# Optimization experiments

Hardware: AMD Instinct MI355X
Metric: run time of the kernel (lower is better)

## Reference

```python
import jax, jax.numpy as jnp
import numpy as np

B, S, D, H, DFF, V, LAT, L = 64, 256, 512, 8, 2048, 128, 512, 6
MAXLEN = 256
NEG = -1e9
EPS = 1e-5


def setup_inputs() -> dict:
    key = jax.random.key(0)
    ks = jax.random.split(key, 32)
    s = 0.02
    rn = lambda k, shape: jax.random.normal(k, shape, jnp.float32) * s
    inp = {
        "z": jax.random.normal(ks[0], (B, LAT), jnp.float32),
        "tgt_seq": jax.random.randint(ks[1], (B, S), 0, V),
        "emb": rn(ks[2], (V, D)).at[0].set(0.0),  # padding_idx=0 row zeroed
        "pos": rn(ks[3], (MAXLEN, D)),
        "proj_w": rn(ks[4], (D, LAT)),
        "proj_b": jnp.zeros((D,), jnp.float32),
        "sa_w": rn(ks[5], (L, 3 * D, D)),
        "sa_b": jnp.zeros((L, 3 * D), jnp.float32),
        "sa_ow": rn(ks[6], (L, D, D)),
        "sa_ob": jnp.zeros((L, D), jnp.float32),
        "ca_w": rn(ks[7], (L, 3 * D, D)),
        "ca_b": jnp.zeros((L, 3 * D), jnp.float32),
        "ca_ow": rn(ks[8], (L, D, D)),
        "ca_ob": jnp.zeros((L, D), jnp.float32),
        "ln1_s": jnp.ones((L, D), jnp.float32),
        "ln1_b": jnp.zeros((L, D), jnp.float32),
        "ln2_s": jnp.ones((L, D), jnp.float32),
        "ln2_b": jnp.zeros((L, D), jnp.float32),
        "ln3_s": jnp.ones((L, D), jnp.float32),
        "ln3_b": jnp.zeros((L, D), jnp.float32),
        "ff1_w": rn(ks[9], (L, DFF, D)),
        "ff1_b": jnp.zeros((L, DFF), jnp.float32),
        "ff2_w": rn(ks[10], (L, D, DFF)),
        "ff2_b": jnp.zeros((L, D), jnp.float32),
        "fc_w": rn(ks[11], (V, D)),
        "fc_b": jnp.zeros((V,), jnp.float32),
    }
    return inp


def _ln(x, s, b):
    m = jnp.mean(x, -1, keepdims=True)
    v = jnp.mean(jnp.square(x - m), -1, keepdims=True)
    return (x - m) * jax.lax.rsqrt(v + EPS) * s + b


def _mha(q_in, k_in, v_in, w, b, ow, ob, mask=None):
    # torch MultiheadAttention: packed in_proj [3D, D], out_proj [D, D]
    wq, wk, wv = w[:D], w[D:2 * D], w[2 * D:]
    bq, bk, bv = b[:D], b[D:2 * D], b[2 * D:]
    dh = D // H
    split = lambda t: t.reshape(t.shape[0], t.shape[1], H, dh)
    q = split(q_in @ wq.T + bq)  # [B,Sq,H,dh]
    k = split(k_in @ wk.T + bk)  # [B,Sk,H,dh]
    v = split(v_in @ wv.T + bv)
    scores = jnp.einsum("bqhd,bkhd->bhqk", q, k) / np.sqrt(dh).astype(np.float32)
    if mask is not None:
        scores = scores + mask
    attn = jax.nn.softmax(scores, axis=-1)
    out = jnp.einsum("bhqk,bkhd->bqhd", attn, v).reshape(q_in.shape[0], q_in.shape[1], D)
    return out @ ow.T + ob


def reference(z, tgt_seq, emb, pos, proj_w, proj_b, sa_w, sa_b, sa_ow, sa_ob,
              ca_w, ca_b, ca_ow, ca_ob, ln1_s, ln1_b, ln2_s, ln2_b, ln3_s, ln3_b,
              ff1_w, ff1_b, ff2_w, ff2_b, fc_w, fc_b):
    # memory = proj(z), length-1 cross-attention memory: [B,1,D]
    mem = (z @ proj_w.T + proj_b)[:, None, :]
    seq_len = tgt_seq.shape[1]
    x = emb[tgt_seq] + pos[:seq_len][None]  # [B,S,D]
    causal = jnp.where(jnp.tril(jnp.ones((seq_len, seq_len), bool)), 0.0, NEG)
    for i in range(L):  # post-norm TransformerDecoderLayer (torch default)
        sa = _mha(x, x, x, sa_w[i], sa_b[i], sa_ow[i], sa_ob[i], causal)
        x = _ln(x + sa, ln1_s[i], ln1_b[i])
        ca = _mha(x, mem, mem, ca_w[i], ca_b[i], ca_ow[i], ca_ob[i])
        x = _ln(x + ca, ln2_s[i], ln2_b[i])
        ff = jax.nn.relu(x @ ff1_w[i].T + ff1_b[i]) @ ff2_w[i].T + ff2_b[i]
        x = _ln(x + ff, ln3_s[i], ln3_b[i])
    logits = x @ fc_w.T + fc_b  # [B,S,V]
    return logits
```

## Files before the change

### kernel.cpp

```cpp
#include <hip/hip_runtime.h>

typedef unsigned int uint;
typedef unsigned short ushort;

typedef __attribute__((ext_vector_type(8))) __bf16 bf16x8;
typedef __attribute__((ext_vector_type(4))) float f32x4;

#define B_ 64
#define S_ 256
#define D_ 512
#define H_ 8
#define DFF_ 2048
#define V_ 128
#define L_ 6
#define BS_ (B_ * S_)

__device__ __forceinline__ float blo(uint u) { return __uint_as_float(u << 16); }
__device__ __forceinline__ float bhi(uint u) { return __uint_as_float(u & 0xffff0000u); }
__device__ __forceinline__ float b2f(ushort u) { return __uint_as_float(((uint)u) << 16); }
__device__ __forceinline__ ushort f2b(float f) {
  uint u = __float_as_uint(f);
  return (ushort)((u + 0x7fffu + ((u >> 16) & 1u)) >> 16);
}
__device__ __forceinline__ uint pack2(float a, float b) {
  return (uint)f2b(a) | ((uint)f2b(b) << 16);
}

#define GLOAD16(gp, lp)                                                        \
  __builtin_amdgcn_global_load_lds(                                            \
      (const __attribute__((address_space(1))) void*)(gp),                     \
      (__attribute__((address_space(3))) void*)(lp), 16, 0, 0)

__global__ __launch_bounds__(256) void conv_kernel(const float* __restrict__ src,
                                                   ushort* __restrict__ dst) {
  size_t p = (size_t)blockIdx.x * 256 + threadIdx.x;
  float2 v = ((const float2*)src)[p];
  ((uint*)dst)[p] = pack2(v.x, v.y);
}

__global__ __launch_bounds__(256) void embed_kernel(
    const int* __restrict__ tgt, const float* __restrict__ emb,
    const float* __restrict__ pos, ushort* __restrict__ x16) {
  int p = blockIdx.x * 256 + threadIdx.x;
  int row = p >> 8;
  int d2 = p & 255;
  int s = row & (S_ - 1);
  int tok = tgt[row];
  float2 e = ((const float2*)emb)[tok * 256 + d2];
  float2 pp = ((const float2*)pos)[s * 256 + d2];
  ((uint*)x16)[p] = pack2(e.x + pp.x, e.y + pp.y);
}

template <int MODE>
__global__ __launch_bounds__(256) void gemm_bt(
    const ushort* __restrict__ A, const ushort* __restrict__ W,
    const float* __restrict__ bias, void* __restrict__ Cv, int N, int K,
    int As, int Ws, int Cs) {
  __shared__ ushort la[128 * 32];
  __shared__ ushort lb[128 * 32];
  const int tid = threadIdx.x;
  const int wv = tid >> 6, lane = tid & 63;
  const int m0 = blockIdx.y << 7, n0 = blockIdx.x << 7;
  const int wm = (wv >> 1) << 6, wn = (wv & 1) << 6;
  const int tr = lane & 15, tq = lane >> 4;

  const int lin0 = wv * 1024 + lane * 8;
  const int lin1 = lin0 + 512;
  const int am0 = lin0 >> 5, ac0 = lin0 & 31;
  const int am1 = lin1 >> 5, ac1 = lin1 & 31;

  const ushort* pa0 = A + (size_t)(m0 + am0) * As + ac0;
  const ushort* pa1 = A + (size_t)(m0 + am1) * As + ac1;
  const ushort* pb0 = W + (size_t)(n0 + am0) * Ws + ac0;
  const ushort* pb1 = W + (size_t)(n0 + am1) * Ws + ac1;
  ushort* la0 = &la[wv * 1024];
  ushort* la1 = &la[wv * 1024 + 512];
  ushort* lb0 = &lb[wv * 1024];
  ushort* lb1 = &lb[wv * 1024 + 512];

  f32x4 acc[4][4];
#pragma unroll
  for (int i = 0; i < 4; ++i)
#pragma unroll
    for (int j = 0; j < 4; ++j) acc[i][j] = (f32x4)(0.f);

  const int KT = K >> 5;
  for (int kt = 0; kt < KT; ++kt) {
    const int kb = kt << 5;
    GLOAD16(pa0 + kb, la0);
    GLOAD16(pa1 + kb, la1);
    GLOAD16(pb0 + kb, lb0);
    GLOAD16(pb1 + kb, lb1);
    __syncthreads();
    bf16x8 av[4], bv[4];
#pragma unroll
    for (int i = 0; i < 4; ++i)
      av[i] = *(const bf16x8*)&la[(wm + i * 16 + tr) * 32 + tq * 8];
#pragma unroll
    for (int j = 0; j < 4; ++j)
      bv[j] = *(const bf16x8*)&lb[(wn + j * 16 + tr) * 32 + tq * 8];
#pragma unroll
    for (int i = 0; i < 4; ++i)
#pragma unroll
      for (int j = 0; j < 4; ++j)
        acc[i][j] =
            __builtin_amdgcn_mfma_f32_16x16x32_bf16(av[i], bv[j], acc[i][j], 0, 0, 0);
    __syncthreads();
  }

#pragma unroll
  for (int j = 0; j < 4; ++j) {
    const int gn = n0 + wn + j * 16 + tr;
    float bj = 0.f;
    if (MODE != 2) bj = bias[gn];
    float scl = 1.f;
    if (MODE == 4) scl = (gn < 512) ? 0.18033688011112042f : 1.f;
#pragma unroll
    for (int i = 0; i < 4; ++i) {
      const int gmb = m0 + wm + i * 16 + tq * 4;
#pragma unroll
      for (int r = 0; r < 4; ++r) {
        const size_t idx = (size_t)(gmb + r) * Cs + gn;
        float v = acc[i][j][r] + bj;
        if (MODE == 1) v = fmaxf(v, 0.f);
        if (MODE == 4) v *= scl;
        if (MODE == 3)
          ((float*)Cv)[idx] = v;
        else if (MODE == 2) {
          ushort* C = (ushort*)Cv;
          C[idx] = f2b(b2f(C[idx]) + acc[i][j][r]);
        } else
          ((ushort*)Cv)[idx] = f2b(v);
      }
    }
  }
}

__global__ __launch_bounds__(256) void gemm_btf(
    const ushort* __restrict__ A0, long zA, const float* __restrict__ W0,
    long zW, const float* __restrict__ bias0, long zb, ushort* __restrict__ C0,
    long zC, int N, int K, int As, int Ws, int Cs) {
  const int zz = blockIdx.z;
  const ushort* A = A0 + zA * zz;
  const float* W = W0 + zW * zz;
  const float* bias = bias0 + zb * zz;
  ushort* C = C0 + zC * zz;

  __shared__ ushort la[128 * 32];
  __shared__ ushort lb[128 * 32];
  const int tid = threadIdx.x;
  const int wv = tid >> 6, lane = tid & 63;
  const int m0 = blockIdx.y << 7, n0 = blockIdx.x << 7;
  const int wm = (wv >> 1) << 6, wn = (wv & 1) << 6;
  const int tr = lane & 15, tq = lane >> 4;

  const int lin0 = wv * 1024 + lane * 8;
  const int lin1 = lin0 + 512;
  const int am0 = lin0 >> 5, ac0 = lin0 & 31;
  const int am1 = lin1 >> 5, ac1 = lin1 & 31;

  const ushort* pa0 = A + (size_t)(m0 + am0) * As + ac0;
  const ushort* pa1 = A + (size_t)(m0 + am1) * As + ac1;
  const float* pb0 = W + (size_t)(n0 + am0) * Ws + ac0;
  const float* pb1 = W + (size_t)(n0 + am1) * Ws + ac1;

  f32x4 acc[4][4];
#pragma unroll
  for (int i = 0; i < 4; ++i)
#pragma unroll
    for (int j = 0; j < 4; ++j) acc[i][j] = (f32x4)(0.f);

  const int KT = K >> 5;
  for (int kt = 0; kt < KT; ++kt) {
    const int kb = kt << 5;
    uint4 ra0 = *(const uint4*)(pa0 + kb);
    uint4 ra1 = *(const uint4*)(pa1 + kb);
    float4 f00 = *(const float4*)(pb0 + kb);
    float4 f01 = *(const float4*)(pb0 + kb + 4);
    float4 f10 = *(const float4*)(pb1 + kb);
    float4 f11 = *(const float4*)(pb1 + kb + 4);
    uint4 rb0 = make_uint4(pack2(f00.x, f00.y), pack2(f00.z, f00.w),
                           pack2(f01.x, f01.y), pack2(f01.z, f01.w));
    uint4 rb1 = make_uint4(pack2(f10.x, f10.y), pack2(f10.z, f10.w),
                           pack2(f11.x, f11.y), pack2(f11.z, f11.w));
    __syncthreads();
    *(uint4*)&la[lin0] = ra0;
    *(uint4*)&la[lin1] = ra1;
    *(uint4*)&lb[lin0] = rb0;
    *(uint4*)&lb[lin1] = rb1;
    __syncthreads();
    bf16x8 av[4], bv[4];
#pragma unroll
    for (int i = 0; i < 4; ++i)
      av[i] = *(const bf16x8*)&la[(wm + i * 16 + tr) * 32 + tq * 8];
#pragma unroll
    for (int j = 0; j < 4; ++j)
      bv[j] = *(const bf16x8*)&lb[(wn + j * 16 + tr) * 32 + tq * 8];
#pragma unroll
    for (int i = 0; i < 4; ++i)
#pragma unroll
      for (int j = 0; j < 4; ++j)
        acc[i][j] =
            __builtin_amdgcn_mfma_f32_16x16x32_bf16(av[i], bv[j], acc[i][j], 0, 0, 0);
  }

#pragma unroll
  for (int j = 0; j < 4; ++j) {
    const int gn = n0 + wn + j * 16 + tr;
    const float bj = bias[gn];
#pragma unroll
    for (int i = 0; i < 4; ++i) {
      const int gmb = m0 + wm + i * 16 + tq * 4;
#pragma unroll
      for (int r = 0; r < 4; ++r)
        C[(size_t)(gmb + r) * Cs + gn] = f2b(acc[i][j][r] + bj);
    }
  }
}

__global__ __launch_bounds__(128) void attn_mfma(ushort* __restrict__ qkv) {
  __shared__ ushort lk[64 * 72];
  __shared__ ushort lvT[64 * 72];
  __shared__ ushort lp[2 * 64 * 72];
  const int qp = blockIdx.x, h = blockIdx.y, b = blockIdx.z;
  const int tid = threadIdx.x;
  const int g = tid >> 6, lane = tid & 63;
  const int tr = lane & 15, tq = lane >> 4;
  const int qc = qp * 2 + g;
  const int q0 = qc << 6;
  ushort* myp = &lp[g * 64 * 72];

  bf16x8 qf[4][2];
#pragma unroll
  for (int i = 0; i < 4; ++i)
#pragma unroll
    for (int s = 0; s < 2; ++s)
      qf[i][s] = *(const bf16x8*)(qkv +
                                  (size_t)(b * 256 + q0 + i * 16 + tr) * 1536 +
                                  h * 64 + s * 32 + tq * 8);

  f32x4 o[4][4];
  float pl[4][4];
#pragma unroll
  for (int i = 0; i < 4; ++i)
#pragma unroll
    for (int j = 0; j < 4; ++j) {
      o[i][j] = (f32x4)(0.f);
      pl[i][j] = 0.f;
    }

  const int key = tid >> 1, half = tid & 1;
  const int cmax = qp * 2 + 1;
  for (int c = 0; c <= cmax; ++c) {
    __syncthreads();
    const ushort* gk =
        qkv + (size_t)(b * 256 + c * 64 + key) * 1536 + 512 + h * 64 + half * 32;
#pragma unroll
    for (int u = 0; u < 4; ++u)
      *(uint4*)&lk[key * 72 + half * 32 + u * 8] = *(const uint4*)(gk + u * 8);
    ushort vloc[32];
#pragma unroll
    for (int u = 0; u < 4; ++u)
      *(uint4*)&vloc[u * 8] = *(const uint4*)(gk + 512 + u * 8);
#pragma unroll
    for (int dd = 0; dd < 32; ++dd)
      lvT[(half * 32 + dd) * 72 + key] = vloc[dd];
    __syncthreads();

    if (c <= qc) {
      f32x4 Sv[4][4];
#pragma unroll
      for (int i = 0; i < 4; ++i)
#pragma unroll
        for (int j = 0; j < 4; ++j) Sv[i][j] = (f32x4)(0.f);
      bf16x8 kf[4][2];
#pragma unroll
      for (int j = 0; j < 4; ++j)
#pragma unroll
        for (int s = 0; s < 2; ++s)
          kf[j][s] = *(const bf16x8*)&lk[(j * 16 + tr) * 72 + s * 32 + tq * 8];
#pragma unroll
      for (int i = 0; i < 4; ++i)
#pragma unroll
        for (int j = 0; j < 4; ++j) {
          Sv[i][j] = __builtin_amdgcn_mfma_f32_16x16x32_bf16(qf[i][0], kf[j][0],
                                                             Sv[i][j], 0, 0, 0);
          Sv[i][j] = __builtin_amdgcn_mfma_f32_16x16x32_bf16(qf[i][1], kf[j][1],
                                                             Sv[i][j], 0, 0, 0);
        }
      const bool diag = (c == qc);
#pragma unroll
      for (int i = 0; i < 4; ++i)
#pragma unroll
        for (int j = 0; j < 4; ++j)
#pragma unroll
          for (int r = 0; r < 4; ++r) {
            float e = exp2f(Sv[i][j][r]);
            if (diag && (j * 16 + tr) > (i * 16 + tq * 4 + r)) e = 0.f;
            pl[i][r] += e;
            myp[(i * 16 + tq * 4 + r) * 72 + j * 16 + tr] =
                (ushort)(__float_as_uint(e) >> 16);
          }
#pragma unroll
      for (int s = 0; s < 2; ++s) {
        bf16x8 vf[4], af[4];
#pragma unroll
        for (int jn = 0; jn < 4; ++jn)
          vf[jn] = *(const bf16x8*)&lvT[(jn * 16 + tr) * 72 + s * 32 + tq * 8];
#pragma unroll
        for (int im = 0; im < 4; ++im)
          af[im] = *(const bf16x8*)&myp[(im * 16 + tr) * 72 + s * 32 + tq * 8];
#pragma unroll
        for (int im = 0; im < 4; ++im)
#pragma unroll
          for (int jn = 0; jn < 4; ++jn)
            o[im][jn] = __builtin_amdgcn_mfma_f32_16x16x32_bf16(af[im], vf[jn],
                                                                o[im][jn], 0, 0, 0);
      }
    }
  }

#pragma unroll
  for (int i = 0; i < 4; ++i)
#pragma unroll
    for (int r = 0; r < 4; ++r) {
      float v = pl[i][r];
      v += __shfl_xor(v, 1, 64);
      v += __shfl_xor(v, 2, 64);
      v += __shfl_xor(v, 4, 64);
      v += __shfl_xor(v, 8, 64);
      pl[i][r] = 1.f / v;
    }

#pragma unroll
  for (int i = 0; i < 4; ++i)
#pragma unroll
    for (int j = 0; j < 4; ++j)
#pragma unroll
      for (int r = 0; r < 4; ++r)
        qkv[(size_t)(b * 256 + q0 + i * 16 + tq * 4 + r) * 1536 + h * 64 +
            j * 16 + tr] = f2b(o[i][j][r] * pl[i][r]);
}

__global__ __launch_bounds__(256) void ln12_kernel(
    ushort* __restrict__ x16, const uint* __restrict__ d1,
    const uint* __restrict__ cavec, const float* __restrict__ s1,
    const float* __restrict__ b1, const float* __restrict__ s2,
    const float* __restrict__ b2p) {
  const int r = blockIdx.x, t = threadIdx.x;
  const int lane = t & 63, wv = t >> 6;
  uint* xr = (uint*)x16 + (size_t)r * 256;
  uint xu = xr[t];
  uint du = d1[(size_t)r * 768 + t];
  float v0 = blo(xu) + blo(du), v1 = bhi(xu) + bhi(du);
  __shared__ float redA[4][2], redB[4][2];
  float sm = v0 + v1, sq = v0 * v0 + v1 * v1;
#pragma unroll
  for (int o = 32; o > 0; o >>= 1) {
    sm += __shfl_xor(sm, o, 64);
    sq += __shfl_xor(sq, o, 64);
  }
  if (lane == 0) {
    redA[wv][0] = sm;
    redA[wv][1] = sq;
  }
  __syncthreads();
  sm = redA[0][0] + redA[1][0] + redA[2][0] + redA[3][0];
  sq = redA[0][1] + redA[1][1] + redA[2][1] + redA[3][1];
  float mean = sm * (1.f / 512.f);
  float var = sq * (1.f / 512.f) - mean * mean;
  float rs = rsqrtf(var + 1e-5f);
  float2 sa = ((const float2*)s1)[t];
  float2 ba = ((const float2*)b1)[t];
  uint cu = cavec[(size_t)(r >> 8) * 256 + t];
  float w0 = (v0 - mean) * rs * sa.x + ba.x + blo(cu);
  float w1 = (v1 - mean) * rs * sa.y + ba.y + bhi(cu);
  sm = w0 + w1;
  sq = w0 * w0 + w1 * w1;
#pragma unroll
  for (int o = 32; o > 0; o >>= 1) {
    sm += __shfl_xor(sm, o, 64);
    sq += __shfl_xor(sq, o, 64);
  }
  if (lane == 0) {
    redB[wv][0] = sm;
    redB[wv][1] = sq;
  }
  __syncthreads();
  sm = redB[0][0] + redB[1][0] + redB[2][0] + redB[3][0];
  sq = redB[0][1] + redB[1][1] + redB[2][1] + redB[3][1];
  mean = sm * (1.f / 512.f);
  var = sq * (1.f / 512.f) - mean * mean;
  rs = rsqrtf(var + 1e-5f);
  float2 sb = ((const float2*)s2)[t];
  float2 bb = ((const float2*)b2p)[t];
  float y0 = (w0 - mean) * rs * sb.x + bb.x;
  float y1 = (w1 - mean) * rs * sb.y + bb.y;
  xr[t] = pack2(y0, y1);
}

__global__ __launch_bounds__(256) void ln_kernel(
    ushort* __restrict__ x16, const uint* __restrict__ delta, int DsU,
    const float* __restrict__ sc, const float* __restrict__ bi) {
  const int r = blockIdx.x, t = threadIdx.x;
  const int lane = t & 63, wv = t >> 6;
  uint* xr = (uint*)x16 + (size_t)r * 256;
  uint xu = xr[t];
  uint du = delta[(size_t)r * DsU + t];
  float v0 = blo(xu) + blo(du), v1 = bhi(xu) + bhi(du);
  float sm = v0 + v1, sq = v0 * v0 + v1 * v1;
#pragma unroll
  for (int o = 32; o > 0; o >>= 1) {
    sm += __shfl_xor(sm, o, 64);
    sq += __shfl_xor(sq, o, 64);
  }
  __shared__ float red[4][2];
  if (lane == 0) {
    red[wv][0] = sm;
    red[wv][1] = sq;
  }
  __syncthreads();
  sm = red[0][0] + red[1][0] + red[2][0] + red[3][0];
  sq = red[0][1] + red[1][1] + red[2][1] + red[3][1];
  float mean = sm * (1.f / 512.f);
  float var = sq * (1.f / 512.f) - mean * mean;
  float rs = rsqrtf(var + 1e-5f);
  float2 s2 = ((const float2*)sc)[t];
  float2 b2 = ((const float2*)bi)[t];
  float y0 = (v0 - mean) * rs * s2.x + b2.x;
  float y1 = (v1 - mean) * rs * s2.y + b2.y;
  xr[t] = pack2(y0, y1);
}

extern "C" void kernel_launch(void* const* d_in, const int* in_sizes, int n_in,
                              void* d_out, int out_size, void* d_ws,
                              size_t ws_size, hipStream_t stream) {
  (void)in_sizes; (void)n_in; (void)out_size; (void)ws_size;
  const float* z = (const float*)d_in[0];
  const int* tgt = (const int*)d_in[1];
  const float* emb = (const float*)d_in[2];
  const float* pos = (const float*)d_in[3];
  const float* projw = (const float*)d_in[4];
  const float* projb = (const float*)d_in[5];
  const float* saw = (const float*)d_in[6];
  const float* sab = (const float*)d_in[7];
  const float* saow = (const float*)d_in[8];
  const float* saob = (const float*)d_in[9];
  const float* caw = (const float*)d_in[10];
  const float* cab = (const float*)d_in[11];
  const float* caow = (const float*)d_in[12];
  const float* caob = (const float*)d_in[13];
  const float* ln1s = (const float*)d_in[14];
  const float* ln1b = (const float*)d_in[15];
  const float* ln2s = (const float*)d_in[16];
  const float* ln2b = (const float*)d_in[17];
  const float* ln3s = (const float*)d_in[18];
  const float* ln3b = (const float*)d_in[19];
  const float* ff1w = (const float*)d_in[20];
  const float* ff1b = (const float*)d_in[21];
  const float* ff2w = (const float*)d_in[22];
  const float* ff2b = (const float*)d_in[23];
  const float* fcw = (const float*)d_in[24];
  const float* fcb = (const float*)d_in[25];

  char* w8 = (char*)d_ws;
  ushort* x16 = (ushort*)w8;
  ushort* qkv = (ushort*)(w8 + (16u << 20));
  ushort* hbuf = qkv;
  ushort* fdel = (ushort*)(w8 + (48u << 20));
  ushort* z16 = (ushort*)(w8 + (64u << 20));
  ushort* memv16 = z16 + 128 * 512;
  ushort* cav16 = memv16 + 128 * 512;
  ushort* cavec16 = cav16 + (size_t)L_ * 128 * 512;
  ushort* wsaw = (ushort*)(w8 + (66u << 20));
  ushort* wsaow = wsaw + (size_t)L_ * 1536 * 512;
  ushort* wff1 = wsaow + (size_t)L_ * 512 * 512;
  ushort* wff2 = wff1 + (size_t)L_ * 2048 * 512;
  ushort* wfcw = wff2 + (size_t)L_ * 512 * 2048;

  conv_kernel<<<(L_ * 1536 * 512) / 512, 256, 0, stream>>>(saw, wsaw);
  conv_kernel<<<(L_ * 512 * 512) / 512, 256, 0, stream>>>(saow, wsaow);
  conv_kernel<<<(L_ * 2048 * 512) / 512, 256, 0, stream>>>(ff1w, wff1);
  conv_kernel<<<(L_ * 512 * 2048) / 512, 256, 0, stream>>>(ff2w, wff2);
  conv_kernel<<<(V_ * 512) / 512, 256, 0, stream>>>(fcw, wfcw);
  conv_kernel<<<(B_ * 512) / 512, 256, 0, stream>>>(z, z16);

  embed_kernel<<<16384, 256, 0, stream>>>(tgt, emb, pos, x16);

  gemm_btf<<<dim3(4, 1, 1), 256, 0, stream>>>(z16, 0, projw, 0, projb, 0,
                                              memv16, 0, 512, 512, 512, 512, 512);
  gemm_btf<<<dim3(4, 1, L_), 256, 0, stream>>>(
      memv16, 0, caw + 1024 * 512, (long)1536 * 512, cab + 1024, 1536, cav16,
      (long)128 * 512, 512, 512, 512, 512, 512);
  gemm_btf<<<dim3(4, 1, L_), 256, 0, stream>>>(
      cav16, (long)128 * 512, caow, (long)512 * 512, caob, 512, cavec16,
      (long)128 * 512, 512, 512, 512, 512, 512);

  for (int i = 0; i < L_; ++i) {
    gemm_bt<4><<<dim3(12, 128), 256, 0, stream>>>(
        x16, wsaw + (size_t)i * 1536 * 512, sab + i * 1536, qkv, 1536, 512, 512,
        512, 1536);
    attn_mfma<<<dim3(2, H_, B_), 128, 0, stream>>>(qkv);
    gemm_bt<0><<<dim3(4, 128), 256, 0, stream>>>(
        qkv, wsaow + (size_t)i * 512 * 512, saob + i * 512, qkv + 512, 512, 512,
        1536, 512, 1536);
    ln12_kernel<<<16384, 256, 0, stream>>>(
        x16, (const uint*)(qkv + 512), (const uint*)(cavec16 + (size_t)i * 128 * 512),
        ln1s + i * 512, ln1b + i * 512, ln2s + i * 512, ln2b + i * 512);
    gemm_bt<1><<<dim3(8, 128), 256, 0, stream>>>(
        x16, wff1 + (size_t)i * 2048 * 512, ff1b + i * 2048, hbuf, 1024, 512,
        512, 512, 1024);
    gemm_bt<0><<<dim3(4, 128), 256, 0, stream>>>(
        hbuf, wff2 + (size_t)i * 512 * 2048, ff2b + i * 512, fdel, 512, 1024,
        1024, 2048, 512);
    gemm_bt<1><<<dim3(8, 128), 256, 0, stream>>>(
        x16, wff1 + ((size_t)i * 2048 + 1024) * 512, ff1b + i * 2048 + 1024,
        hbuf, 1024, 512, 512, 512, 1024);
    gemm_bt<2><<<dim3(4, 128), 256, 0, stream>>>(
        hbuf, wff2 + (size_t)i * 512 * 2048 + 1024, (const float*)0, fdel, 512,
        1024, 1024, 2048, 512);
    ln_kernel<<<16384, 256, 0, stream>>>(x16, (const uint*)fdel, 256,
                                         ln3s + i * 512, ln3b + i * 512);
  }
  gemm_bt<3><<<dim3(1, 128), 256, 0, stream>>>(x16, wfcw, fcb, d_out, 128, 512,
                                               512, 512, 128);
}
```

Measured before the change: 1.924 ms.

## Add 256x256-tile bf16 GEMM with 4-stage LDS pipeline for layer matmuls

Adds a new 512-thread GEMM kernel that computes 256x256 output tiles, replacing the 128x128 gemm_bt for the QKV, out-projection and FFN matmuls. Operands are loaded straight into LDS through a 4-deep ring of buffers with a swizzled layout, and s_setprio is raised around the MFMA blocks. The epilogue goes through LDS so global stores are coalesced. Each tile reuses more data per load, but it needs about 136KB of dynamic LDS per block and produces far fewer blocks (128 to 384 per GEMM), which may leave some CUs idle.

```diff
diff --git a/kernel.cpp b/kernel.cpp
--- a/kernel.cpp
+++ b/kernel.cpp
@@ -30,6 +30,14 @@
   __builtin_amdgcn_global_load_lds(                                            \
       (const __attribute__((address_space(1))) void*)(gp),                     \
       (__attribute__((address_space(3))) void*)(lp), 16, 0, 0)
+
+#define BARX()                                                                 \
+  do {                                                                         \
+    asm volatile("" ::: "memory");                                             \
+    __builtin_amdgcn_s_barrier();                                              \
+    asm volatile("" ::: "memory");                                             \
+  } while (0)
+#define WAITV(N) asm volatile("s_waitcnt vmcnt(" #N ")" ::: "memory")
 
 __global__ __launch_bounds__(256) void conv_kernel(const float* __restrict__ src,
                                                    ushort* __restrict__ dst) {
@@ -49,6 +57,144 @@
   float2 e = ((const float2*)emb)[tok * 256 + d2];
   float2 pp = ((const float2*)pos)[s * 256 + d2];
   ((uint*)x16)[p] = pack2(e.x + pp.x, e.y + pp.y);
+}
+
+template <int MODE>
+__global__ __launch_bounds__(512) void gemm256(
+    const ushort* __restrict__ A, const ushort* __restrict__ W,
+    const float* __restrict__ bias, ushort* __restrict__ C, int N, int K,
+    int As, int Ws, int Cs) {
+  extern __shared__ ushort shl[];
+  const int tid = threadIdx.x;
+  const int wv = tid >> 6, lane = tid & 63;
+  const int tr = lane & 15, tq = lane >> 4;
+  const int wm = wv >> 2, wn = wv & 3;
+  const int m0 = blockIdx.y << 8, n0 = blockIdx.x << 8;
+
+  const int rr = tid >> 2;
+  const int cswz = ((tid & 3) * 8) ^ (((tid >> 5) & 1) << 4);
+  const ushort* gA0 = A + (size_t)(m0 + rr) * As + cswz;
+  const ushort* gA1 = A + (size_t)(m0 + 128 + rr) * As + cswz;
+  const ushort* gB0 = W + (size_t)(n0 + rr) * Ws + cswz;
+  const ushort* gB1 = W + (size_t)(n0 + 128 + rr) * Ws + cswz;
+
+  const int cu = (tq * 8) ^ ((tr >> 3) << 4);
+  const int aoff = (wm * 128 + tr) * 32 + cu;
+  const int boff = (wn * 64 + tr) * 32 + cu;
+
+  f32x4 acc[8][4];
+#pragma unroll
+  for (int i = 0; i < 8; ++i)
+#pragma unroll
+    for (int j = 0; j < 4; ++j) acc[i][j] = (f32x4)(0.f);
+
+  const int NT = K >> 5;
+
+#define STG_A(t)                                                               \
+  do {                                                                         \
+    ushort* d_ = shl + (((t) & 3) << 14) + wv * 512;                           \
+    GLOAD16(gA0 + (t) * 32, d_);                                               \
+    GLOAD16(gA1 + (t) * 32, d_ + 4096);                                        \
+  } while (0)
+#define STG_B(t)                                                               \
+  do {                                                                         \
+    ushort* d_ = shl + (((t) & 3) << 14) + 8192 + wv * 512;                    \
+    GLOAD16(gB0 + (t) * 32, d_);                                               \
+    GLOAD16(gB1 + (t) * 32, d_ + 4096);                                        \
+  } while (0)
+
+  STG_A(0); STG_B(0);
+  STG_A(1); STG_B(1);
+  STG_A(2); STG_B(2);
+  WAITV(8);
+  BARX();
+
+  for (int t = 0; t < NT; ++t) {
+    const ushort* sA = shl + ((t & 3) << 14);
+    const ushort* sB = sA + 8192;
+    bf16x8 bv[4], av[4];
+#pragma unroll
+    for (int j = 0; j < 4; ++j) bv[j] = *(const bf16x8*)&sB[boff + j * 512];
+#pragma unroll
+    for (int i = 0; i < 4; ++i) av[i] = *(const bf16x8*)&sA[aoff + i * 512];
+    if (t + 3 < NT) STG_A(t + 3);
+    BARX();
+    __builtin_amdgcn_s_setprio(1);
+#pragma unroll
+    for (int i = 0; i < 4; ++i)
+#pragma unroll
+      for (int j = 0; j < 4; ++j)
+        acc[i][j] = __builtin_amdgcn_mfma_f32_16x16x32_bf16(bv[j], av[i],
+                                                            acc[i][j], 0, 0, 0);
+    __builtin_amdgcn_s_setprio(0);
+    BARX();
+#pragma unroll
+    for (int i = 0; i < 4; ++i)
+      av[i] = *(const bf16x8*)&sA[aoff + (i + 4) * 512];
+    if (t + 3 < NT) STG_B(t + 3);
+    BARX();
+    __builtin_amdgcn_s_setprio(1);
+#pragma unroll
+    for (int i = 0; i < 4; ++i)
+#pragma unroll
+      for (int j = 0; j < 4; ++j)
+        acc[i + 4][j] = __builtin_amdgcn_mfma_f32_16x16x32_bf16(
+            bv[j], av[i], acc[i + 4][j], 0, 0, 0);
+    __builtin_amdgcn_s_setprio(0);
+    if (t + 3 < NT) {
+      WAITV(8);
+    } else if (t + 2 < NT) {
+      WAITV(4);
+    } else {
+      WAITV(0);
+    }
+    BARX();
+  }
+#undef STG_A
+#undef STG_B
+
+#pragma unroll
+  for (int i = 0; i < 8; ++i)
+#pragma unroll
+    for (int j = 0; j < 4; ++j) {
+      const int gn4 = n0 + wn * 64 + j * 16 + tq * 4;
+      float b0 = 0.f, b1 = 0.f, b2 = 0.f, b3 = 0.f;
+      if (MODE != 2) {
+        float4 bb = ((const float4*)bias)[gn4 >> 2];
+        b0 = bb.x; b1 = bb.y; b2 = bb.z; b3 = bb.w;
+      }
+      float v0 = acc[i][j][0] + b0, v1 = acc[i][j][1] + b1,
+            v2 = acc[i][j][2] + b2, v3 = acc[i][j][3] + b3;
+      if (MODE == 1) {
+        v0 = fmaxf(v0, 0.f); v1 = fmaxf(v1, 0.f);
+        v2 = fmaxf(v2, 0.f); v3 = fmaxf(v3, 0.f);
+      }
+      if (MODE == 4) {
+        const float scl = (gn4 < 512) ? 0.18033688011112042f : 1.f;
+        v0 *= scl; v1 *= scl; v2 *= scl; v3 *= scl;
+      }
+      uint2 pk;
+      pk.x = pack2(v0, v1);
+      pk.y = pack2(v2, v3);
+      *(uint2*)&shl[(wm * 128 + i * 16 + tr) * 272 + wn * 64 + j * 16 +
+                    tq * 4] = pk;
+    }
+  BARX();
+#pragma unroll
+  for (int u = 0; u < 16; ++u) {
+    const int f = u * 512 + tid;
+    const int row = f >> 5, sl = f & 31;
+    uint4 val = *(const uint4*)&shl[row * 272 + sl * 8];
+    ushort* gp = C + (size_t)(m0 + row) * Cs + n0 + sl * 8;
+    if (MODE == 2) {
+      uint4 c = *(const uint4*)gp;
+      val.x = pack2(blo(val.x) + blo(c.x), bhi(val.x) + bhi(c.x));
+      val.y = pack2(blo(val.y) + blo(c.y), bhi(val.y) + bhi(c.y));
+      val.z = pack2(blo(val.z) + blo(c.z), bhi(val.z) + bhi(c.z));
+      val.w = pack2(blo(val.w) + blo(c.w), bhi(val.w) + bhi(c.w));
+    }
+    *(uint4*)gp = val;
+  }
 }
 
 template <int MODE>
@@ -463,6 +609,20 @@
   const float* fcw = (const float*)d_in[24];
   const float* fcb = (const float*)d_in[25];
 
+  const int SHB = 139264;
+  static bool s_attr = false;
+  if (!s_attr) {
+    s_attr = true;
+    (void)hipFuncSetAttribute(reinterpret_cast<const void*>(gemm256<0>),
+                              hipFuncAttributeMaxDynamicSharedMemorySize, SHB);
+    (void)hipFuncSetAttribute(reinterpret_cast<const void*>(gemm256<1>),
+                              hipFuncAttributeMaxDynamicSharedMemorySize, SHB);
+    (void)hipFuncSetAttribute(reinterpret_cast<const void*>(gemm256<2>),
+                              hipFuncAttributeMaxDynamicSharedMemorySize, SHB);
+    (void)hipFuncSetAttribute(reinterpret_cast<const void*>(gemm256<4>),
+                              hipFuncAttributeMaxDynamicSharedMemorySize, SHB);
+  }
+
   char* w8 = (char*)d_ws;
   ushort* x16 = (ushort*)w8;
   ushort* qkv = (ushort*)(w8 + (16u << 20));
@@ -497,26 +657,26 @@
       (long)128 * 512, 512, 512, 512, 512, 512);
 
   for (int i = 0; i < L_; ++i) {
-    gemm_bt<4><<<dim3(12, 128), 256, 0, stream>>>(
-        x16, wsaw + (size_t)i * 1536 * 512, sab + i * 1536, qkv, 1536, 512, 512,
-        512, 1536);
+    gemm256<4><<<dim3(6, 64), 512, SHB, stream>>>(
+        x16, wsaw + (size_t)i * 1536 * 512, sab + i * 1536, qkv, 1536, 512,
+        512, 512, 1536);
     attn_mfma<<<dim3(2, H_, B_), 128, 0, stream>>>(qkv);
-    gemm_bt<0><<<dim3(4, 128), 256, 0, stream>>>(
-        qkv, wsaow + (size_t)i * 512 * 512, saob + i * 512, qkv + 512, 512, 512,
-        1536, 512, 1536);
+    gemm256<0><<<dim3(2, 64), 512, SHB, stream>>>(
+        qkv, wsaow + (size_t)i * 512 * 512, saob + i * 512, qkv + 512, 512,
+        512, 1536, 512, 1536);
     ln12_kernel<<<16384, 256, 0, stream>>>(
         x16, (const uint*)(qkv + 512), (const uint*)(cavec16 + (size_t)i * 128 * 512),
         ln1s + i * 512, ln1b + i * 512, ln2s + i * 512, ln2b + i * 512);
-    gemm_bt<1><<<dim3(8, 128), 256, 0, stream>>>(
+    gemm256<1><<<dim3(4, 64), 512, SHB, stream>>>(
         x16, wff1 + (size_t)i * 2048 * 512, ff1b + i * 2048, hbuf, 1024, 512,
         512, 512, 1024);
-    gemm_bt<0><<<dim3(4, 128), 256, 0, stream>>>(
+    gemm256<0><<<dim3(2, 64), 512, SHB, stream>>>(
         hbuf, wff2 + (size_t)i * 512 * 2048, ff2b + i * 512, fdel, 512, 1024,
         1024, 2048, 512);
-    gemm_bt<1><<<dim3(8, 128), 256, 0, stream>>>(
+    gemm256<1><<<dim3(4, 64), 512, SHB, stream>>>(
         x16, wff1 + ((size_t)i * 2048 + 1024) * 512, ff1b + i * 2048 + 1024,
         hbuf, 1024, 512, 512, 512, 1024);
-    gemm_bt<2><<<dim3(4, 128), 256, 0, stream>>>(
+    gemm256<2><<<dim3(2, 64), 512, SHB, stream>>>(
         hbuf, wff2 + (size_t)i * 512 * 2048 + 1024, (const float*)0, fdel, 512,
         1024, 1024, 2048, 512);
     ln_kernel<<<16384, 256, 0, stream>>>(x16, (const uint*)fdel, 256,
```

Result: no change. 1.898 ms (-1.3%).
